# Kernel tuning notes

Hardware: AMD Instinct MI355X
Metric: run time of the kernel (lower is better)

Reference implementation:

```python
import jax, jax.numpy as jnp
import numpy as np
from jax import lax

B, T, L = 256, 512, 128


def setup_inputs() -> dict:
    key = jax.random.key(0)
    k1, k2, k3 = jax.random.split(key, 3)
    labels = jax.random.randint(k1, (B, T), 0, L)
    y_true = jax.nn.one_hot(labels, L, dtype=jnp.float32)  # [B,T,L]
    y_pred = jax.random.normal(k2, (B, T, L), dtype=jnp.float32)
    trans = jax.random.normal(k3, (L, L), dtype=jnp.float32) * 0.1
    return {"y_true": y_true, "y_pred": y_pred, "trans": trans}


def reference(y_true, y_pred, trans):
    # ---- log partition via forward algorithm (lax.scan over time) ----
    init = y_pred[:, 0]  # [B,L] initial alpha

    def step(alpha, emit):  # alpha [B,L], emit [B,L]
        # alpha[:, i, None] + trans[i, j] -> logsumexp over previous label i
        new = jax.nn.logsumexp(alpha[:, :, None] + trans[None, :, :], axis=1) + emit
        return new, None

    emits = jnp.swapaxes(y_pred[:, 1:], 0, 1)  # [T-1,B,L]
    final_alpha, _ = lax.scan(step, init, emits)  # [B,L]
    log_norm = jax.nn.logsumexp(final_alpha, axis=1, keepdims=True)  # [B,1]

    # ---- path score (unnormalized log prob of the true path) ----
    point_score = jnp.sum(y_pred * y_true, axis=(1, 2), keepdims=False)[:, None]  # [B,1]
    trans_score = jnp.einsum('bti,btj,ij->b', y_true[:, :-1], y_true[:, 1:], trans)[:, None]  # [B,1]

    return log_norm - (point_score + trans_score)  # [B,1]
```

## Files before the change

kernel.cpp:

```cpp
#include <hip/hip_runtime.h>

typedef float  f32x4 __attribute__((ext_vector_type(4)));
typedef short  s16x8 __attribute__((ext_vector_type(8)));

#define Tt 512
#define Ll 128
#define CH 16
#define CL 32
#define NR 15
#define RUNS 30
#define NSCORE 256

#define WS_PT 0
#define WS_TR 256
#define WS_KR 512
#define WS_KB (512 + 256*NR)
#define WS_RV (512 + 2*256*NR)
#define WS_BV (WS_RV + 256*NR*128)

__device__ __forceinline__ void bar_lgkm() {
  asm volatile("s_waitcnt lgkmcnt(0)" ::: "memory");
  __builtin_amdgcn_s_barrier();
  asm volatile("" ::: "memory");
}
__device__ __forceinline__ ushort bf16rn(float f) {
  unsigned u = __float_as_uint(f);
  u += 0x7FFFu + ((u >> 16) & 1u);
  return (ushort)(u >> 16);
}
__device__ __forceinline__ float bf16tof(ushort h) {
  return __uint_as_float(((unsigned)h) << 16);
}

__global__ __launch_bounds__(512, 1) void crf_chunk(
    const float* __restrict__ yt_g, const float* __restrict__ yp_g,
    const float* __restrict__ tr_g, float* __restrict__ wsf)
{
  __shared__ __align__(16) ushort ubuf[2][16 * 128];
  __shared__ int   lab_s[Tt];
  __shared__ float redp[8], redt[8];

  const int tid = threadIdx.x, wv = tid >> 6, l = tid & 63;

  if (blockIdx.x < NSCORE) {
    const int b = blockIdx.x;
    const float4* yp4 = (const float4*)(yp_g + (size_t)b * Tt * Ll);
    const float4* yt4 = (const float4*)(yt_g + (size_t)b * Tt * Ll);
    float pt = 0.f;
    #pragma unroll 4
    for (int i = 0; i < 32; ++i) {
      int f = tid + i * 512;
      float4 a = yp4[f], y = yt4[f];
      pt += a.x * y.x + a.y * y.y + a.z * y.z + a.w * y.w;
      int t = f >> 5, jb = (f & 31) << 2;
      if (y.x > .5f) lab_s[t] = jb;
      if (y.y > .5f) lab_s[t] = jb + 1;
      if (y.z > .5f) lab_s[t] = jb + 2;
      if (y.w > .5f) lab_s[t] = jb + 3;
    }
    __syncthreads();
    float trl = (tid < Tt - 1) ? tr_g[lab_s[tid] * Ll + lab_s[tid + 1]] : 0.f;
    #pragma unroll
    for (int o = 32; o; o >>= 1) { pt += __shfl_xor(pt, o); trl += __shfl_xor(trl, o); }
    if (l == 0) { redp[wv] = pt; redt[wv] = trl; }
    __syncthreads();
    if (tid == 0) {
      float sp = 0.f, st = 0.f;
      #pragma unroll
      for (int k2 = 0; k2 < 8; ++k2) { sp += redp[k2]; st += redt[k2]; }
      wsf[WS_PT + b] = sp; wsf[WS_TR + b] = st;
    }
    return;
  }

  const int bid2 = blockIdx.x - NSCORE;
  const int g    = bid2 / RUNS, run = bid2 % RUNS;
  const bool FWD = (run < NR);
  const int c    = FWD ? run : (run - NR + 1);
  const int b0   = g * 16;
  const int l15  = l & 15, q = l >> 4;
  const int jg   = (wv << 4) | l15;
  const int swA  = (l15 & 7) << 4;

  const int t_hi = (c == CH - 1) ? (Tt - 1) : (c * CL + CL);
  const int t_lo = c * CL + 1;
  const int n    = FWD ? CL : (t_hi - t_lo + 1);

  s16x8 Bf[4];
  #pragma unroll
  for (int kt = 0; kt < 4; ++kt) {
    s16x8 v;
    #pragma unroll
    for (int e = 0; e < 8; ++e) {
      int k = 32 * kt + 8 * q + e;
      float tv = FWD ? tr_g[k * Ll + l15] : tr_g[l15 * Ll + k];
      v[e] = (short)bf16rn(__expf(tv));
    }
    Bf[kt] = v;
  }

  const size_t ypb0 = ((size_t)(b0 + 4 * q + 0) * Tt) * Ll + jg;
  const size_t ypb1 = ((size_t)(b0 + 4 * q + 1) * Tt) * Ll + jg;
  const size_t ypb2 = ((size_t)(b0 + 4 * q + 2) * Tt) * Ll + jg;
  const size_t ypb3 = ((size_t)(b0 + 4 * q + 3) * Tt) * Ll + jg;

  float K0 = 0.f, K1 = 0.f, K2 = 0.f, K3 = 0.f;
  float res0 = 0.f, res1 = 0.f, res2 = 0.f, res3 = 0.f;

  {
    float iv0, iv1, iv2, iv3;
    if (FWD) {
      if (c == 0) {
        iv0 = __expf(yp_g[ypb0]); iv1 = __expf(yp_g[ypb1]);
        iv2 = __expf(yp_g[ypb2]); iv3 = __expf(yp_g[ypb3]);
      } else { iv0 = iv1 = iv2 = iv3 = 1.f; }
    } else {
      size_t off = (size_t)t_hi * Ll;
      iv0 = __expf(yp_g[ypb0 + off]); iv1 = __expf(yp_g[ypb1 + off]);
      iv2 = __expf(yp_g[ypb2 + off]); iv3 = __expf(yp_g[ypb3 + off]);
    }
    char* wb = (char*)ubuf;
    *(ushort*)(wb + (4*q+0)*256 + ((2*jg) ^ (((4*q+0)&7)<<4))) = bf16rn(iv0);
    *(ushort*)(wb + (4*q+1)*256 + ((2*jg) ^ (((4*q+1)&7)<<4))) = bf16rn(iv1);
    *(ushort*)(wb + (4*q+2)*256 + ((2*jg) ^ (((4*q+2)&7)<<4))) = bf16rn(iv2);
    *(ushort*)(wb + (4*q+3)*256 + ((2*jg) ^ (((4*q+3)&7)<<4))) = bf16rn(iv3);
  }

  float PEa0, PEa1, PEa2, PEa3, PEb0, PEb1, PEb2, PEb3;
  {
    size_t o0 = (size_t)(FWD ? t_lo : (t_hi - 1)) * Ll;
    PEa0 = yp_g[ypb0+o0]; PEa1 = yp_g[ypb1+o0]; PEa2 = yp_g[ypb2+o0]; PEa3 = yp_g[ypb3+o0];
    size_t o1 = (size_t)(FWD ? (t_lo + 1) : (t_hi - 2)) * Ll;
    PEb0 = yp_g[ypb0+o1]; PEb1 = yp_g[ypb1+o1]; PEb2 = yp_g[ypb2+o1]; PEb3 = yp_g[ypb3+o1];
  }
  bar_lgkm();

#define ITER(K_, PE0,PE1,PE2,PE3)                                             \
  {                                                                           \
    const int cur = (K_) & 1;                                                 \
    const char* abase = (const char*)ubuf + cur * 4096 + l15 * 256;           \
    f32x4 dd = {0.f, 0.f, 0.f, 0.f};                                          \
    _Pragma("unroll")                                                         \
    for (int kt = 0; kt < 4; ++kt) {                                          \
      float4 af = *(const float4*)(abase + ((64 * kt + 16 * q) ^ swA));       \
      dd = __builtin_amdgcn_mfma_f32_16x16x32_bf16(*(const s16x8*)&af,        \
             Bf[kt], dd, 0, 0, 0);                                            \
    }                                                                         \
    const bool last = (K_) == n - 1;                                          \
    const bool ren  = (((K_) & 7) == 7);                                      \
    float wex0 = __expf(PE0), wex1 = __expf(PE1),                             \
          wex2 = __expf(PE2), wex3 = __expf(PE3);                             \
    float rn0 = 1.f, rn1 = 1.f, rn2 = 1.f, rn3 = 1.f;                         \
    if (ren) {                                                                \
      const char* pb = (const char*)ubuf + cur * 4096;                        \
      float p0 = bf16tof(*(const ushort*)(pb + (4*q+0)*256 + (((4*q+0)&7)<<4))); \
      float p1 = bf16tof(*(const ushort*)(pb + (4*q+1)*256 + (((4*q+1)&7)<<4))); \
      float p2 = bf16tof(*(const ushort*)(pb + (4*q+2)*256 + (((4*q+2)&7)<<4))); \
      float p3 = bf16tof(*(const ushort*)(pb + (4*q+3)*256 + (((4*q+3)&7)<<4))); \
      K0 += __logf(p0); K1 += __logf(p1); K2 += __logf(p2); K3 += __logf(p3); \
      rn0 = 1.f / p0; rn1 = 1.f / p1; rn2 = 1.f / p2; rn3 = 1.f / p3;         \
    }                                                                         \
    float v0 = dd[0], v1 = dd[1], v2 = dd[2], v3 = dd[3];                     \
    if (!(!FWD && last)) { v0 *= wex0; v1 *= wex1; v2 *= wex2; v3 *= wex3; }  \
    if (ren) { v0 *= rn0; v1 *= rn1; v2 *= rn2; v3 *= rn3; }                  \
    if (last) { res0 = v0; res1 = v1; res2 = v2; res3 = v3; }                 \
    else {                                                                    \
      char* wb = (char*)ubuf + (cur ^ 1) * 4096;                              \
      *(ushort*)(wb + (4*q+0)*256 + ((2*jg) ^ (((4*q+0)&7)<<4))) = bf16rn(v0);\
      *(ushort*)(wb + (4*q+1)*256 + ((2*jg) ^ (((4*q+1)&7)<<4))) = bf16rn(v1);\
      *(ushort*)(wb + (4*q+2)*256 + ((2*jg) ^ (((4*q+2)&7)<<4))) = bf16rn(v2);\
      *(ushort*)(wb + (4*q+3)*256 + ((2*jg) ^ (((4*q+3)&7)<<4))) = bf16rn(v3);\
    }                                                                         \
    if ((K_) + 2 < n) {                                                       \
      const size_t o2 = (size_t)(FWD ? (t_lo + (K_) + 2)                      \
                                     : (t_hi - (K_) - 3)) * Ll;               \
      PE0 = yp_g[ypb0+o2]; PE1 = yp_g[ypb1+o2];                               \
      PE2 = yp_g[ypb2+o2]; PE3 = yp_g[ypb3+o2];                               \
    }                                                                         \
    bar_lgkm();                                                               \
  }

  for (int k = 0; k < n; k += 2) {
    ITER(k, PEa0, PEa1, PEa2, PEa3)
    if (k + 1 < n) {
      ITER(k + 1, PEb0, PEb1, PEb2, PEb3)
    }
  }
#undef ITER

  {
    const int cs = FWD ? c : (c - 1);
    float* rp = wsf + (FWD ? WS_RV : WS_BV);
    rp[((size_t)(b0 + 4*q + 0) * NR + cs) * 128 + jg] = res0;
    rp[((size_t)(b0 + 4*q + 1) * NR + cs) * 128 + jg] = res1;
    rp[((size_t)(b0 + 4*q + 2) * NR + cs) * 128 + jg] = res2;
    rp[((size_t)(b0 + 4*q + 3) * NR + cs) * 128 + jg] = res3;
    if (wv == 0 && l15 == 0) {
      float* kp = wsf + (FWD ? WS_KR : WS_KB);
      kp[(b0 + 4*q + 0) * NR + cs] = K0;
      kp[(b0 + 4*q + 1) * NR + cs] = K1;
      kp[(b0 + 4*q + 2) * NR + cs] = K2;
      kp[(b0 + 4*q + 3) * NR + cs] = K3;
    }
  }
}

__global__ __launch_bounds__(64) void crf_stitch(
    const float* __restrict__ wsf, float* __restrict__ out)
{
  const int b = blockIdx.x, j = threadIdx.x;
  const float* RV = wsf + WS_RV + (size_t)b * NR * 128;
  const float* BV = wsf + WS_BV + (size_t)b * NR * 128;
  const float* Kr = wsf + WS_KR + b * NR;
  const float* Kb = wsf + WS_KB + b * NR;
  float lz;
  {
    float d = RV[j] * BV[j] + RV[j + 64] * BV[j + 64];
    #pragma unroll
    for (int o = 32; o; o >>= 1) d += __shfl_xor(d, o);
    lz = __logf(d) + Kr[0] + Kb[0];
  }
  #pragma unroll
  for (int cc = 1; cc < NR; ++cc) {
    float d = RV[cc*128 + j] * BV[cc*128 + j] + RV[cc*128 + j + 64] * BV[cc*128 + j + 64];
    float s = RV[cc*128 + j] + RV[cc*128 + j + 64];
    #pragma unroll
    for (int o = 32; o; o >>= 1) { d += __shfl_xor(d, o); s += __shfl_xor(s, o); }
    lz += __logf(d) - __logf(s) + Kb[cc];
  }
  if (j == 0) out[b] = lz - wsf[WS_PT + b] - wsf[WS_TR + b];
}

extern "C" void kernel_launch(void* const* d_in, const int* in_sizes, int n_in,
                              void* d_out, int out_size, void* d_ws, size_t ws_size,
                              hipStream_t stream) {
  const float* y_true = (const float*)d_in[0];
  const float* y_pred = (const float*)d_in[1];
  const float* trans  = (const float*)d_in[2];
  float* out = (float*)d_out;
  float* wsf = (float*)d_ws;
  crf_chunk<<<dim3(NSCORE + 16 * RUNS), dim3(512), 0, stream>>>(y_true, y_pred, trans, wsf);
  crf_stitch<<<dim3(256), dim3(64), 0, stream>>>(wsf, out);
}
```

Before: 65.79 us.

## Halve chunk length and use 256-thread blocks computing two column tiles per wave

Time chunks are halved (32 chunks of 16 steps), which doubles the number of forward/backward runs and shortens the serial dependency chain per block. Blocks shrink to 256 threads (4 waves); each wave now issues two MFMAs per k-tile to cover 128 output labels, with two sets of transition fragments held in registers. Launch bounds allow several blocks per CU. The intent is to cut the serial latency of the scan by using more parallel chunks, at the cost of more stitch work, more workspace traffic, and more registers per thread.

```diff
diff --git a/kernel.cpp b/kernel.cpp
--- a/kernel.cpp
+++ b/kernel.cpp
@@ -5,10 +5,10 @@
 
 #define Tt 512
 #define Ll 128
-#define CH 16
-#define CL 32
-#define NR 15
-#define RUNS 30
+#define CH 32
+#define CL 16
+#define NR 31
+#define RUNS 62
 #define NSCORE 256
 
 #define WS_PT 0
@@ -32,13 +32,15 @@
   return __uint_as_float(((unsigned)h) << 16);
 }
 
-__global__ __launch_bounds__(512, 1) void crf_chunk(
+__global__ __attribute__((amdgpu_flat_work_group_size(256, 256),
+                          amdgpu_waves_per_eu(2, 4)))
+void crf_chunk(
     const float* __restrict__ yt_g, const float* __restrict__ yp_g,
     const float* __restrict__ tr_g, float* __restrict__ wsf)
 {
   __shared__ __align__(16) ushort ubuf[2][16 * 128];
   __shared__ int   lab_s[Tt];
-  __shared__ float redp[8], redt[8];
+  __shared__ float redp[4], redt[4];
 
   const int tid = threadIdx.x, wv = tid >> 6, l = tid & 63;
 
@@ -48,8 +50,8 @@
     const float4* yt4 = (const float4*)(yt_g + (size_t)b * Tt * Ll);
     float pt = 0.f;
     #pragma unroll 4
-    for (int i = 0; i < 32; ++i) {
-      int f = tid + i * 512;
+    for (int i = 0; i < 64; ++i) {
+      int f = tid + i * 256;
       float4 a = yp4[f], y = yt4[f];
       pt += a.x * y.x + a.y * y.y + a.z * y.z + a.w * y.w;
       int t = f >> 5, jb = (f & 31) << 2;
@@ -59,16 +61,16 @@
       if (y.w > .5f) lab_s[t] = jb + 3;
     }
     __syncthreads();
-    float trl = (tid < Tt - 1) ? tr_g[lab_s[tid] * Ll + lab_s[tid + 1]] : 0.f;
+    float trl = 0.f;
+    for (int tt0 = tid; tt0 < Tt - 1; tt0 += 256)
+      trl += tr_g[lab_s[tt0] * Ll + lab_s[tt0 + 1]];
     #pragma unroll
     for (int o = 32; o; o >>= 1) { pt += __shfl_xor(pt, o); trl += __shfl_xor(trl, o); }
     if (l == 0) { redp[wv] = pt; redt[wv] = trl; }
     __syncthreads();
     if (tid == 0) {
-      float sp = 0.f, st = 0.f;
-      #pragma unroll
-      for (int k2 = 0; k2 < 8; ++k2) { sp += redp[k2]; st += redt[k2]; }
-      wsf[WS_PT + b] = sp; wsf[WS_TR + b] = st;
+      wsf[WS_PT + b] = redp[0] + redp[1] + redp[2] + redp[3];
+      wsf[WS_TR + b] = redt[0] + redt[1] + redt[2] + redt[3];
     }
     return;
   }
@@ -79,122 +81,152 @@
   const int c    = FWD ? run : (run - NR + 1);
   const int b0   = g * 16;
   const int l15  = l & 15, q = l >> 4;
-  const int jg   = (wv << 4) | l15;
+  const int jg0  = (wv << 4) | l15;
+  const int jg1  = jg0 + 64;
   const int swA  = (l15 & 7) << 4;
 
   const int t_hi = (c == CH - 1) ? (Tt - 1) : (c * CL + CL);
   const int t_lo = c * CL + 1;
   const int n    = FWD ? CL : (t_hi - t_lo + 1);
 
-  s16x8 Bf[4];
+  s16x8 BfA[4], BfB[4];
   #pragma unroll
   for (int kt = 0; kt < 4; ++kt) {
-    s16x8 v;
+    s16x8 va, vb;
     #pragma unroll
     for (int e = 0; e < 8; ++e) {
       int k = 32 * kt + 8 * q + e;
-      float tv = FWD ? tr_g[k * Ll + l15] : tr_g[l15 * Ll + k];
-      v[e] = (short)bf16rn(__expf(tv));
-    }
-    Bf[kt] = v;
-  }
-
-  const size_t ypb0 = ((size_t)(b0 + 4 * q + 0) * Tt) * Ll + jg;
-  const size_t ypb1 = ((size_t)(b0 + 4 * q + 1) * Tt) * Ll + jg;
-  const size_t ypb2 = ((size_t)(b0 + 4 * q + 2) * Tt) * Ll + jg;
-  const size_t ypb3 = ((size_t)(b0 + 4 * q + 3) * Tt) * Ll + jg;
+      float ta = FWD ? tr_g[k * Ll + jg0] : tr_g[jg0 * Ll + k];
+      float tb = FWD ? tr_g[k * Ll + jg1] : tr_g[jg1 * Ll + k];
+      va[e] = (short)bf16rn(__expf(ta));
+      vb[e] = (short)bf16rn(__expf(tb));
+    }
+    BfA[kt] = va; BfB[kt] = vb;
+  }
+
+  const size_t ypb0 = ((size_t)(b0 + 4 * q + 0) * Tt) * Ll + jg0;
+  const size_t ypb1 = ((size_t)(b0 + 4 * q + 1) * Tt) * Ll + jg0;
+  const size_t ypb2 = ((size_t)(b0 + 4 * q + 2) * Tt) * Ll + jg0;
+  const size_t ypb3 = ((size_t)(b0 + 4 * q + 3) * Tt) * Ll + jg0;
 
   float K0 = 0.f, K1 = 0.f, K2 = 0.f, K3 = 0.f;
-  float res0 = 0.f, res1 = 0.f, res2 = 0.f, res3 = 0.f;
-
-  {
-    float iv0, iv1, iv2, iv3;
-    if (FWD) {
-      if (c == 0) {
-        iv0 = __expf(yp_g[ypb0]); iv1 = __expf(yp_g[ypb1]);
-        iv2 = __expf(yp_g[ypb2]); iv3 = __expf(yp_g[ypb3]);
-      } else { iv0 = iv1 = iv2 = iv3 = 1.f; }
+  float rA0 = 0.f, rA1 = 0.f, rA2 = 0.f, rA3 = 0.f;
+  float rB0 = 0.f, rB1 = 0.f, rB2 = 0.f, rB3 = 0.f;
+
+#define SWZ(B_) (((B_) & 7) << 4)
+#define WRT(BUF, M_, JG, V_) \
+  *(ushort*)((char*)ubuf + (BUF) * 4096 + (4*q+(M_))*256 + ((2*(JG)) ^ SWZ(4*q+(M_)))) = bf16rn(V_)
+
+  {
+    float a0, a1, a2, a3, bb0, bb1, bb2, bb3;
+    if (FWD && c != 0) {
+      a0 = a1 = a2 = a3 = bb0 = bb1 = bb2 = bb3 = 1.f;
     } else {
-      size_t off = (size_t)t_hi * Ll;
-      iv0 = __expf(yp_g[ypb0 + off]); iv1 = __expf(yp_g[ypb1 + off]);
-      iv2 = __expf(yp_g[ypb2 + off]); iv3 = __expf(yp_g[ypb3 + off]);
-    }
-    char* wb = (char*)ubuf;
-    *(ushort*)(wb + (4*q+0)*256 + ((2*jg) ^ (((4*q+0)&7)<<4))) = bf16rn(iv0);
-    *(ushort*)(wb + (4*q+1)*256 + ((2*jg) ^ (((4*q+1)&7)<<4))) = bf16rn(iv1);
-    *(ushort*)(wb + (4*q+2)*256 + ((2*jg) ^ (((4*q+2)&7)<<4))) = bf16rn(iv2);
-    *(ushort*)(wb + (4*q+3)*256 + ((2*jg) ^ (((4*q+3)&7)<<4))) = bf16rn(iv3);
-  }
-
-  float PEa0, PEa1, PEa2, PEa3, PEb0, PEb1, PEb2, PEb3;
+      size_t off = FWD ? 0 : (size_t)t_hi * Ll;
+      a0  = __expf(yp_g[ypb0 + off]); a1  = __expf(yp_g[ypb1 + off]);
+      a2  = __expf(yp_g[ypb2 + off]); a3  = __expf(yp_g[ypb3 + off]);
+      bb0 = __expf(yp_g[ypb0 + off + 64]); bb1 = __expf(yp_g[ypb1 + off + 64]);
+      bb2 = __expf(yp_g[ypb2 + off + 64]); bb3 = __expf(yp_g[ypb3 + off + 64]);
+    }
+    WRT(0, 0, jg0, a0); WRT(0, 1, jg0, a1); WRT(0, 2, jg0, a2); WRT(0, 3, jg0, a3);
+    WRT(0, 0, jg1, bb0); WRT(0, 1, jg1, bb1); WRT(0, 2, jg1, bb2); WRT(0, 3, jg1, bb3);
+  }
+
+  float EAa0, EAa1, EAa2, EAa3, EBa0, EBa1, EBa2, EBa3;
+  float EAb0, EAb1, EAb2, EAb3, EBb0, EBb1, EBb2, EBb3;
   {
     size_t o0 = (size_t)(FWD ? t_lo : (t_hi - 1)) * Ll;
-    PEa0 = yp_g[ypb0+o0]; PEa1 = yp_g[ypb1+o0]; PEa2 = yp_g[ypb2+o0]; PEa3 = yp_g[ypb3+o0];
+    EAa0 = yp_g[ypb0+o0];    EAa1 = yp_g[ypb1+o0];
+    EAa2 = yp_g[ypb2+o0];    EAa3 = yp_g[ypb3+o0];
+    EBa0 = yp_g[ypb0+o0+64]; EBa1 = yp_g[ypb1+o0+64];
+    EBa2 = yp_g[ypb2+o0+64]; EBa3 = yp_g[ypb3+o0+64];
     size_t o1 = (size_t)(FWD ? (t_lo + 1) : (t_hi - 2)) * Ll;
-    PEb0 = yp_g[ypb0+o1]; PEb1 = yp_g[ypb1+o1]; PEb2 = yp_g[ypb2+o1]; PEb3 = yp_g[ypb3+o1];
+    EAb0 = yp_g[ypb0+o1];    EAb1 = yp_g[ypb1+o1];
+    EAb2 = yp_g[ypb2+o1];    EAb3 = yp_g[ypb3+o1];
+    EBb0 = yp_g[ypb0+o1+64]; EBb1 = yp_g[ypb1+o1+64];
+    EBb2 = yp_g[ypb2+o1+64]; EBb3 = yp_g[ypb3+o1+64];
   }
   bar_lgkm();
 
-#define ITER(K_, PE0,PE1,PE2,PE3)                                             \
+#define ITER(K_, A0,A1,A2,A3, B0,B1,B2,B3)                                    \
   {                                                                           \
     const int cur = (K_) & 1;                                                 \
     const char* abase = (const char*)ubuf + cur * 4096 + l15 * 256;           \
-    f32x4 dd = {0.f, 0.f, 0.f, 0.f};                                          \
+    f32x4 dd0 = {0.f,0.f,0.f,0.f}, dd1 = {0.f,0.f,0.f,0.f};                   \
     _Pragma("unroll")                                                         \
     for (int kt = 0; kt < 4; ++kt) {                                          \
       float4 af = *(const float4*)(abase + ((64 * kt + 16 * q) ^ swA));       \
-      dd = __builtin_amdgcn_mfma_f32_16x16x32_bf16(*(const s16x8*)&af,        \
-             Bf[kt], dd, 0, 0, 0);                                            \
+      dd0 = __builtin_amdgcn_mfma_f32_16x16x32_bf16(*(const s16x8*)&af,       \
+              BfA[kt], dd0, 0, 0, 0);                                         \
+      dd1 = __builtin_amdgcn_mfma_f32_16x16x32_bf16(*(const s16x8*)&af,       \
+              BfB[kt], dd1, 0, 0, 0);                                         \
     }                                                                         \
     const bool last = (K_) == n - 1;                                          \
     const bool ren  = (((K_) & 7) == 7);                                      \
-    float wex0 = __expf(PE0), wex1 = __expf(PE1),                             \
-          wex2 = __expf(PE2), wex3 = __expf(PE3);                             \
+    float wA0 = __expf(A0), wA1 = __expf(A1), wA2 = __expf(A2), wA3 = __expf(A3); \
+    float wB0 = __expf(B0), wB1 = __expf(B1), wB2 = __expf(B2), wB3 = __expf(B3); \
     float rn0 = 1.f, rn1 = 1.f, rn2 = 1.f, rn3 = 1.f;                         \
     if (ren) {                                                                \
       const char* pb = (const char*)ubuf + cur * 4096;                        \
-      float p0 = bf16tof(*(const ushort*)(pb + (4*q+0)*256 + (((4*q+0)&7)<<4))); \
-      float p1 = bf16tof(*(const ushort*)(pb + (4*q+1)*256 + (((4*q+1)&7)<<4))); \
-      float p2 = bf16tof(*(const ushort*)(pb + (4*q+2)*256 + (((4*q+2)&7)<<4))); \
-      float p3 = bf16tof(*(const ushort*)(pb + (4*q+3)*256 + (((4*q+3)&7)<<4))); \
+      float p0 = bf16tof(*(const ushort*)(pb + (4*q+0)*256 + SWZ(4*q+0)));    \
+      float p1 = bf16tof(*(const ushort*)(pb + (4*q+1)*256 + SWZ(4*q+1)));    \
+      float p2 = bf16tof(*(const ushort*)(pb + (4*q+2)*256 + SWZ(4*q+2)));    \
+      float p3 = bf16tof(*(const ushort*)(pb + (4*q+3)*256 + SWZ(4*q+3)));    \
       K0 += __logf(p0); K1 += __logf(p1); K2 += __logf(p2); K3 += __logf(p3); \
       rn0 = 1.f / p0; rn1 = 1.f / p1; rn2 = 1.f / p2; rn3 = 1.f / p3;         \
     }                                                                         \
-    float v0 = dd[0], v1 = dd[1], v2 = dd[2], v3 = dd[3];                     \
-    if (!(!FWD && last)) { v0 *= wex0; v1 *= wex1; v2 *= wex2; v3 *= wex3; }  \
-    if (ren) { v0 *= rn0; v1 *= rn1; v2 *= rn2; v3 *= rn3; }                  \
-    if (last) { res0 = v0; res1 = v1; res2 = v2; res3 = v3; }                 \
-    else {                                                                    \
-      char* wb = (char*)ubuf + (cur ^ 1) * 4096;                              \
-      *(ushort*)(wb + (4*q+0)*256 + ((2*jg) ^ (((4*q+0)&7)<<4))) = bf16rn(v0);\
-      *(ushort*)(wb + (4*q+1)*256 + ((2*jg) ^ (((4*q+1)&7)<<4))) = bf16rn(v1);\
-      *(ushort*)(wb + (4*q+2)*256 + ((2*jg) ^ (((4*q+2)&7)<<4))) = bf16rn(v2);\
-      *(ushort*)(wb + (4*q+3)*256 + ((2*jg) ^ (((4*q+3)&7)<<4))) = bf16rn(v3);\
+    float v0 = dd0[0], v1 = dd0[1], v2 = dd0[2], v3 = dd0[3];                 \
+    float u0 = dd1[0], u1 = dd1[1], u2 = dd1[2], u3 = dd1[3];                 \
+    if (!(!FWD && last)) {                                                    \
+      v0 *= wA0; v1 *= wA1; v2 *= wA2; v3 *= wA3;                             \
+      u0 *= wB0; u1 *= wB1; u2 *= wB2; u3 *= wB3;                             \
+    }                                                                         \
+    if (ren) {                                                                \
+      v0 *= rn0; v1 *= rn1; v2 *= rn2; v3 *= rn3;                             \
+      u0 *= rn0; u1 *= rn1; u2 *= rn2; u3 *= rn3;                             \
+    }                                                                         \
+    if (last) {                                                               \
+      rA0 = v0; rA1 = v1; rA2 = v2; rA3 = v3;                                 \
+      rB0 = u0; rB1 = u1; rB2 = u2; rB3 = u3;                                 \
+    } else {                                                                  \
+      const int nb = cur ^ 1;                                                 \
+      WRT(nb, 0, jg0, v0); WRT(nb, 1, jg0, v1);                               \
+      WRT(nb, 2, jg0, v2); WRT(nb, 3, jg0, v3);                               \
+      WRT(nb, 0, jg1, u0); WRT(nb, 1, jg1, u1);                               \
+      WRT(nb, 2, jg1, u2); WRT(nb, 3, jg1, u3);                               \
     }                                                                         \
     if ((K_) + 2 < n) {                                                       \
       const size_t o2 = (size_t)(FWD ? (t_lo + (K_) + 2)                      \
                                      : (t_hi - (K_) - 3)) * Ll;               \
-      PE0 = yp_g[ypb0+o2]; PE1 = yp_g[ypb1+o2];                               \
-      PE2 = yp_g[ypb2+o2]; PE3 = yp_g[ypb3+o2];                               \
+      A0 = yp_g[ypb0+o2];    A1 = yp_g[ypb1+o2];                              \
+      A2 = yp_g[ypb2+o2];    A3 = yp_g[ypb3+o2];                              \
+      B0 = yp_g[ypb0+o2+64]; B1 = yp_g[ypb1+o2+64];                           \
+      B2 = yp_g[ypb2+o2+64]; B3 = yp_g[ypb3+o2+64];                           \
     }                                                                         \
     bar_lgkm();                                                               \
   }
 
   for (int k = 0; k < n; k += 2) {
-    ITER(k, PEa0, PEa1, PEa2, PEa3)
+    ITER(k, EAa0,EAa1,EAa2,EAa3, EBa0,EBa1,EBa2,EBa3)
     if (k + 1 < n) {
-      ITER(k + 1, PEb0, PEb1, PEb2, PEb3)
+      ITER(k + 1, EAb0,EAb1,EAb2,EAb3, EBb0,EBb1,EBb2,EBb3)
     }
   }
 #undef ITER
+#undef WRT
+#undef SWZ
 
   {
     const int cs = FWD ? c : (c - 1);
     float* rp = wsf + (FWD ? WS_RV : WS_BV);
-    rp[((size_t)(b0 + 4*q + 0) * NR + cs) * 128 + jg] = res0;
-    rp[((size_t)(b0 + 4*q + 1) * NR + cs) * 128 + jg] = res1;
-    rp[((size_t)(b0 + 4*q + 2) * NR + cs) * 128 + jg] = res2;
-    rp[((size_t)(b0 + 4*q + 3) * NR + cs) * 128 + jg] = res3;
+    rp[((size_t)(b0 + 4*q + 0) * NR + cs) * 128 + jg0] = rA0;
+    rp[((size_t)(b0 + 4*q + 1) * NR + cs) * 128 + jg0] = rA1;
+    rp[((size_t)(b0 + 4*q + 2) * NR + cs) * 128 + jg0] = rA2;
+    rp[((size_t)(b0 + 4*q + 3) * NR + cs) * 128 + jg0] = rA3;
+    rp[((size_t)(b0 + 4*q + 0) * NR + cs) * 128 + jg1] = rB0;
+    rp[((size_t)(b0 + 4*q + 1) * NR + cs) * 128 + jg1] = rB1;
+    rp[((size_t)(b0 + 4*q + 2) * NR + cs) * 128 + jg1] = rB2;
+    rp[((size_t)(b0 + 4*q + 3) * NR + cs) * 128 + jg1] = rB3;
     if (wv == 0 && l15 == 0) {
       float* kp = wsf + (FWD ? WS_KR : WS_KB);
       kp[(b0 + 4*q + 0) * NR + cs] = K0;
@@ -239,6 +271,6 @@
   const float* trans  = (const float*)d_in[2];
   float* out = (float*)d_out;
   float* wsf = (float*)d_ws;
-  crf_chunk<<<dim3(NSCORE + 16 * RUNS), dim3(512), 0, stream>>>(y_true, y_pred, trans, wsf);
+  crf_chunk<<<dim3(NSCORE + 16 * RUNS), dim3(256), 0, stream>>>(y_true, y_pred, trans, wsf);
   crf_stitch<<<dim3(256), dim3(64), 0, stream>>>(wsf, out);
 }
```

New measurement: 63.78 us. 1.03x faster.
